# Performance work log

Hardware: AMD Instinct MI355X
Metric: run time of the kernel (lower is better)

## Reference

```python
import jax, jax.numpy as jnp
import numpy as np

NUM_HEADS = 32

def setup_inputs() -> dict:
    key = jax.random.key(0)
    ks = jax.random.split(key, 5)
    B, S, D = 2, 2048, 1024
    d = D // NUM_HEADS  # 32
    return {
        "x": jax.random.normal(ks[0], (B, S, D), dtype=jnp.float32),
        "wq": jax.random.normal(ks[1], (d, d), dtype=jnp.float32) / np.sqrt(d),
        "bq": jnp.zeros((d,), dtype=jnp.float32),
        "wk": jax.random.normal(ks[2], (d, d), dtype=jnp.float32) / np.sqrt(d),
        "bk": jnp.zeros((d,), dtype=jnp.float32),
        "wv": jax.random.normal(ks[3], (d, d), dtype=jnp.float32) / np.sqrt(d),
        "bv": jnp.zeros((d,), dtype=jnp.float32),
        "wo": jax.random.normal(ks[4], (D, D), dtype=jnp.float32) / np.sqrt(D),
        "bo": jnp.zeros((D,), dtype=jnp.float32),
    }

def reference(x, wq, bq, wk, bk, wv, bv, wo, bo):
    B, S, D = x.shape
    H = NUM_HEADS
    d = D // H
    # split heads: [B, S, H, d] -> [B, H, S, d]
    h = x.reshape(B, S, H, d).transpose(0, 2, 1, 3)
    # shared per-head Q/K/V projections (single SelfAttention submodule)
    q = jnp.einsum('bhsd,de->bhse', h, wq) + bq
    k = jnp.einsum('bhsd,de->bhse', h, wk) + bk
    v = jnp.einsum('bhsd,de->bhse', h, wv) + bv
    scale = 1.0 / jnp.sqrt(jnp.asarray(d, dtype=x.dtype))
    scores = jnp.einsum('bhqd,bhkd->bhqk', q, k) * scale  # [B,H,S,S]
    attn = jax.nn.softmax(scores, axis=-1)
    out = jnp.einsum('bhqk,bhkd->bhqd', attn, v)  # [B,H,S,d]
    # concat heads -> [B, S, D]
    concat = out.transpose(0, 2, 1, 3).reshape(B, S, D)
    return concat @ wo + bo
```

## Files before the change

kernel.cpp:

```cpp
#include <hip/hip_runtime.h>
#include <hip/hip_bf16.h>

typedef __attribute__((ext_vector_type(8))) short bf16x8;
typedef __attribute__((ext_vector_type(4))) short bf16x4;
typedef __attribute__((ext_vector_type(4))) float f32x4;

#if defined(__has_builtin)
#if __has_builtin(__builtin_amdgcn_exp2f)
#define EXP2F(x) __builtin_amdgcn_exp2f(x)
#else
#define EXP2F(x) exp2f(x)
#endif
#else
#define EXP2F(x) exp2f(x)
#endif

#define S_LEN 2048
#define NH 32
#define HD 32
#define DMODEL 1024
#define NB 2

static __device__ __forceinline__ unsigned int cvt_pk_bf16(float lo, float hi) {
    unsigned int r;
    asm("v_cvt_pk_bf16_f32 %0, %1, %2" : "=v"(r) : "v"(lo), "v"(hi));
    return r;
}

static __device__ __forceinline__ void mfma16_acc(f32x4& d, bf16x4 a, bf16x4 b) {
    asm("s_nop 2\n\tv_mfma_f32_16x16x16_bf16 %0, %1, %2, %0"
        : "+v"(d) : "v"(a), "v"(b));
}

__global__ __launch_bounds__(256) void qkv_mfma(
    const float* __restrict__ x,
    const float* __restrict__ wq, const float* __restrict__ bq,
    const float* __restrict__ wk, const float* __restrict__ bk,
    const float* __restrict__ wv, const float* __restrict__ bv,
    __hip_bfloat16* __restrict__ qws,
    __hip_bfloat16* __restrict__ kws,
    __hip_bfloat16* __restrict__ vtws)
{
    const int tid = threadIdx.x;
    const int w  = tid >> 6;
    const int ln = tid & 63;
    const int lg = ln >> 4, lm = ln & 15;

    const int bi = blockIdx.x;
    const int tb = bi >> 2;
    const int hq = bi & 3;
    const int t0 = tb * 16;
    const int b  = t0 >> 11;
    const int s0 = t0 & 2047;

    const float SC = 0.1767766953f * 1.44269504089f;

    bf16x8 wqB[2], wkB[2], wvA[2];
    f32x4 bqC[2], bkC[2], bvC[2];
#pragma unroll
    for (int et = 0; et < 2; ++et) {
        const int e = et * 16 + lm;
        union { unsigned int u4[4]; bf16x8 v; } tq, tk, tv;
#pragma unroll
        for (int jj = 0; jj < 4; ++jj) {
            int k0 = lg * 8 + jj * 2;
            tq.u4[jj] = cvt_pk_bf16(wq[k0 * 32 + e] * SC, wq[(k0 + 1) * 32 + e] * SC);
            tk.u4[jj] = cvt_pk_bf16(wk[k0 * 32 + e],      wk[(k0 + 1) * 32 + e]);
            tv.u4[jj] = cvt_pk_bf16(wv[k0 * 32 + e],      wv[(k0 + 1) * 32 + e]);
        }
        wqB[et] = tq.v; wkB[et] = tk.v; wvA[et] = tv.v;

        float bqe = bq[e] * SC;
        float bke = bk[e];
        bqC[et] = (f32x4){bqe, bqe, bqe, bqe};
        bkC[et] = (f32x4){bke, bke, bke, bke};
#pragma unroll
        for (int r = 0; r < 4; ++r)
            bvC[et][r] = bv[et * 16 + lg * 4 + r];
    }

#pragma unroll
    for (int u = 0; u < 2; ++u) {
        const int h = hq * 8 + w * 2 + u;

        const float* xp = x + (size_t)(t0 + lm) * DMODEL + h * 32 + lg * 8;
        float4 xlo = *reinterpret_cast<const float4*>(xp);
        float4 xhi = *reinterpret_cast<const float4*>(xp + 4);
        union { unsigned int u4[4]; bf16x8 v; } xa;
        xa.u4[0] = cvt_pk_bf16(xlo.x, xlo.y);
        xa.u4[1] = cvt_pk_bf16(xlo.z, xlo.w);
        xa.u4[2] = cvt_pk_bf16(xhi.x, xhi.y);
        xa.u4[3] = cvt_pk_bf16(xhi.z, xhi.w);

        const int bh = b * NH + h;
        __hip_bfloat16* qrow = qws + ((size_t)bh * S_LEN + s0) * HD;
        __hip_bfloat16* krow = kws + ((size_t)bh * S_LEN + s0) * HD;
        __hip_bfloat16* vrow = vtws + (size_t)bh * HD * S_LEN + s0;

#pragma unroll
        for (int et = 0; et < 2; ++et) {
            f32x4 qd = __builtin_amdgcn_mfma_f32_16x16x32_bf16(xa.v, wqB[et], bqC[et], 0, 0, 0);
            f32x4 kd = __builtin_amdgcn_mfma_f32_16x16x32_bf16(xa.v, wkB[et], bkC[et], 0, 0, 0);
            f32x4 vd = __builtin_amdgcn_mfma_f32_16x16x32_bf16(wvA[et], xa.v, bvC[et], 0, 0, 0);
#pragma unroll
            for (int r = 0; r < 4; ++r) {
                int srow = 4 * lg + r;
                qrow[(size_t)srow * HD + et * 16 + lm] = __float2bfloat16(qd[r]);
                krow[(size_t)srow * HD + et * 16 + lm] = __float2bfloat16(kd[r]);
                vrow[(size_t)(et * 16 + 4 * lg + r) * S_LEN + lm] = __float2bfloat16(vd[r]);
            }
        }
    }
}

__global__ __launch_bounds__(256) void wo_transpose(
    const float* __restrict__ wo, __hip_bfloat16* __restrict__ wot)
{
    __shared__ float t[64][65];
    const int bx = blockIdx.x;
    const int by = blockIdx.y;
    const int tid = threadIdx.x;
    const int col = tid & 63, row4 = tid >> 6;
#pragma unroll
    for (int i = 0; i < 16; ++i) {
        int r = i * 4 + row4;
        t[r][col] = wo[(size_t)(bx * 64 + r) * DMODEL + by * 64 + col];
    }
    __syncthreads();
#pragma unroll
    for (int i = 0; i < 16; ++i) {
        int r = i * 4 + row4;
        wot[(size_t)(by * 64 + r) * DMODEL + bx * 64 + col] =
            __float2bfloat16(t[col][r]);
    }
}

__global__ __launch_bounds__(256) void attn_kernel(
    const __hip_bfloat16* __restrict__ qws,
    const __hip_bfloat16* __restrict__ kws,
    const __hip_bfloat16* __restrict__ vtws,
    __hip_bfloat16* __restrict__ cws)
{
    const int tid = threadIdx.x;
    const int w  = tid >> 6;
    const int ln = tid & 63;
    const int lg = ln >> 4;
    const int lm = ln & 15;

    const int bi  = blockIdx.x;
    const int xcd = bi & 7;
    const int idx = bi >> 3;
    const int qt  = idx & 31;
    const int bh  = (xcd << 3) | (idx >> 5);
    const int b   = bh >> 5;
    const int h   = bh & 31;

    const __hip_bfloat16* qp = qws + (size_t)bh * S_LEN * HD;
    const char* kpb = (const char*)(kws  + (size_t)bh * S_LEN * HD);
    const char* vpb = (const char*)(vtws + (size_t)bh * HD * S_LEN);

    const int qr0 = qt * 64 + w * 16;

    bf16x8 qb = *reinterpret_cast<const bf16x8*>(qp + (size_t)(qr0 + lm) * HD + lg * 8);

    __shared__ __align__(16) char kv[8192];

    f32x4 l4 = {0.f, 0.f, 0.f, 0.f};
    f32x4 o0 = {0.f, 0.f, 0.f, 0.f};
    f32x4 o1 = {0.f, 0.f, 0.f, 0.f};
    const f32x4 zoff = {-8.f, -8.f, -8.f, -8.f};

    const int vrow  = tid >> 3;
    const int vslot = tid & 7;
    const size_t vsrc = (size_t)vrow * (S_LEN * 2) +
                        (size_t)(vslot ^ (vrow & 7)) * 16;

    int voff[4];
#pragma unroll
    for (int c = 0; c < 4; ++c)
        voff[c] = 4096 + lm * 128 + (((2 * c + (lg >> 1)) ^ (lm & 7)) << 4) + (lg & 1) * 8;

    uint4 kreg = *reinterpret_cast<const uint4*>(kpb + tid * 16);
    uint4 vreg = *reinterpret_cast<const uint4*>(vpb + vsrc);

    for (int kt = 0; kt < S_LEN / 64; ++kt) {
        if (kt) __syncthreads();
        *reinterpret_cast<uint4*>(&kv[tid * 16])        = kreg;
        *reinterpret_cast<uint4*>(&kv[4096 + tid * 16]) = vreg;
        __syncthreads();
        if (kt + 1 < S_LEN / 64) {
            kreg = *reinterpret_cast<const uint4*>(
                kpb + (size_t)(kt + 1) * 4096 + tid * 16);
            vreg = *reinterpret_cast<const uint4*>(
                vpb + vsrc + (size_t)(kt + 1) * 128);
        }

        f32x4 s[4];
#pragma unroll
        for (int c = 0; c < 4; ++c) {
            bf16x8 kf = *reinterpret_cast<const bf16x8*>(
                &kv[c * 1024 + lm * 64 + lg * 16]);
            s[c] = __builtin_amdgcn_mfma_f32_16x16x32_bf16(kf, qb, zoff, 0, 0, 0);
        }

        bf16x4 pb[4];
#pragma unroll
        for (int c = 0; c < 4; ++c) {
            float p0 = EXP2F(s[c][0]);
            float p1 = EXP2F(s[c][1]);
            float p2 = EXP2F(s[c][2]);
            float p3 = EXP2F(s[c][3]);
            l4[0] += p0; l4[1] += p1; l4[2] += p2; l4[3] += p3;
            union { unsigned int u[2]; bf16x4 v; } pk_;
            pk_.u[0] = cvt_pk_bf16(p0, p1);
            pk_.u[1] = cvt_pk_bf16(p2, p3);
            pb[c] = pk_.v;
        }

#pragma unroll
        for (int c = 0; c < 4; ++c) {
            bf16x4 va = *reinterpret_cast<const bf16x4*>(&kv[voff[c]]);
            bf16x4 vb = *reinterpret_cast<const bf16x4*>(&kv[voff[c] + 2048]);
            mfma16_acc(o0, va, pb[c]);
            mfma16_acc(o1, vb, pb[c]);
        }
    }

    asm volatile("s_nop 7\n\ts_nop 7");

    float l = (l4[0] + l4[1]) + (l4[2] + l4[3]);
    l += __shfl_xor(l, 16);
    l += __shfl_xor(l, 32);
    float inv = 1.0f / l;

    __hip_bfloat16* cb = cws + ((size_t)b * S_LEN + qr0 + lm) * DMODEL + h * HD;
    union { unsigned int u[2]; bf16x4 v; } w0, w1;
    w0.u[0] = cvt_pk_bf16(o0[0] * inv, o0[1] * inv);
    w0.u[1] = cvt_pk_bf16(o0[2] * inv, o0[3] * inv);
    w1.u[0] = cvt_pk_bf16(o1[0] * inv, o1[1] * inv);
    w1.u[1] = cvt_pk_bf16(o1[2] * inv, o1[3] * inv);
    *reinterpret_cast<bf16x4*>(cb + lg * 4)      = w0.v;
    *reinterpret_cast<bf16x4*>(cb + 16 + lg * 4) = w1.v;
}

__global__ __launch_bounds__(256) void out_gemm(
    const __hip_bfloat16* __restrict__ A,
    const __hip_bfloat16* __restrict__ Bt,
    const float* __restrict__ bo,
    float* __restrict__ out)
{
    const int tid = threadIdx.x;
    const int ln = tid & 63;
    const int w  = tid >> 6;
    const int lg = ln >> 4, lm = ln & 15;
    const int wr = w >> 1, wc = w & 1;
    const int bi = blockIdx.x;
    const int bn = bi & 7;
    const int bm = bi >> 3;
    const int r0 = bm * 64;
    const int n0 = bn * 128;

    __shared__ __align__(16) char lds[24576];

    f32x4 acc[2][4];
#pragma unroll
    for (int m = 0; m < 2; ++m)
#pragma unroll
        for (int n = 0; n < 4; ++n)
            acc[m][n] = {0.f, 0.f, 0.f, 0.f};

    const int srow = tid >> 3;
    const int sj   = tid & 7;
    const int swo  = srow * 128 + ((sj ^ (srow & 7)) << 4);

    const __hip_bfloat16* Ab = A  + (size_t)r0 * DMODEL;
    const __hip_bfloat16* Bb = Bt + (size_t)n0 * DMODEL;

    uint4 ar0 = *reinterpret_cast<const uint4*>(Ab + (size_t)srow        * DMODEL + sj * 8);
    uint4 ar1 = *reinterpret_cast<const uint4*>(Ab + (size_t)(srow + 32) * DMODEL + sj * 8);
    uint4 br0 = *reinterpret_cast<const uint4*>(Bb + (size_t)srow        * DMODEL + sj * 8);
    uint4 br1 = *reinterpret_cast<const uint4*>(Bb + (size_t)(srow + 32) * DMODEL + sj * 8);
    uint4 br2 = *reinterpret_cast<const uint4*>(Bb + (size_t)(srow + 64) * DMODEL + sj * 8);
    uint4 br3 = *reinterpret_cast<const uint4*>(Bb + (size_t)(srow + 96) * DMODEL + sj * 8);

    for (int k0 = 0; k0 < DMODEL; k0 += 64) {
        if (k0) __syncthreads();
        *reinterpret_cast<uint4*>(&lds[swo])          = ar0;
        *reinterpret_cast<uint4*>(&lds[swo + 4096])   = ar1;
        *reinterpret_cast<uint4*>(&lds[8192 + swo])           = br0;
        *reinterpret_cast<uint4*>(&lds[8192 + swo + 4096])    = br1;
        *reinterpret_cast<uint4*>(&lds[8192 + swo + 8192])    = br2;
        *reinterpret_cast<uint4*>(&lds[8192 + swo + 12288])   = br3;
        __syncthreads();
        if (k0 + 64 < DMODEL) {
            const __hip_bfloat16* An = Ab + k0 + 64;
            const __hip_bfloat16* Bn = Bb + k0 + 64;
            ar0 = *reinterpret_cast<const uint4*>(An + (size_t)srow        * DMODEL + sj * 8);
            ar1 = *reinterpret_cast<const uint4*>(An + (size_t)(srow + 32) * DMODEL + sj * 8);
            br0 = *reinterpret_cast<const uint4*>(Bn + (size_t)srow        * DMODEL + sj * 8);
            br1 = *reinterpret_cast<const uint4*>(Bn + (size_t)(srow + 32) * DMODEL + sj * 8);
            br2 = *reinterpret_cast<const uint4*>(Bn + (size_t)(srow + 64) * DMODEL + sj * 8);
            br3 = *reinterpret_cast<const uint4*>(Bn + (size_t)(srow + 96) * DMODEL + sj * 8);
        }

#pragma unroll
        for (int kh = 0; kh < 2; ++kh) {
            bf16x8 af[2], bf[4];
#pragma unroll
            for (int m = 0; m < 2; ++m) {
                int row = wr * 32 + m * 16 + lm;
                af[m] = *reinterpret_cast<const bf16x8*>(
                    &lds[row * 128 + (((kh * 4 + lg) ^ (row & 7)) << 4)]);
            }
#pragma unroll
            for (int n = 0; n < 4; ++n) {
                int row = wc * 64 + n * 16 + lm;
                bf[n] = *reinterpret_cast<const bf16x8*>(
                    &lds[8192 + row * 128 + (((kh * 4 + lg) ^ (row & 7)) << 4)]);
            }
#pragma unroll
            for (int m = 0; m < 2; ++m)
#pragma unroll
                for (int n = 0; n < 4; ++n)
                    acc[m][n] = __builtin_amdgcn_mfma_f32_16x16x32_bf16(
                        af[m], bf[n], acc[m][n], 0, 0, 0);
        }
    }

#pragma unroll
    for (int n = 0; n < 4; ++n) {
        int col = n0 + wc * 64 + n * 16 + lm;
        float bv = bo[col];
#pragma unroll
        for (int m = 0; m < 2; ++m) {
#pragma unroll
            for (int r = 0; r < 4; ++r) {
                int row = r0 + wr * 32 + m * 16 + lg * 4 + r;
                out[(size_t)row * DMODEL + col] = acc[m][n][r] + bv;
            }
        }
    }
}

extern "C" void kernel_launch(void* const* d_in, const int* in_sizes, int n_in,
                              void* d_out, int out_size, void* d_ws, size_t ws_size,
                              hipStream_t stream)
{
    const float* x  = (const float*)d_in[0];
    const float* wq = (const float*)d_in[1];
    const float* bq = (const float*)d_in[2];
    const float* wk = (const float*)d_in[3];
    const float* bk = (const float*)d_in[4];
    const float* wv = (const float*)d_in[5];
    const float* bv = (const float*)d_in[6];
    const float* wo = (const float*)d_in[7];
    const float* bo = (const float*)d_in[8];
    float* out = (float*)d_out;

    char* ws = (char*)d_ws;
    __hip_bfloat16* qws  = (__hip_bfloat16*)(ws);
    __hip_bfloat16* kws  = (__hip_bfloat16*)(ws + ((size_t)8  << 20));
    __hip_bfloat16* vtws = (__hip_bfloat16*)(ws + ((size_t)16 << 20));
    __hip_bfloat16* cws  = (__hip_bfloat16*)(ws + ((size_t)24 << 20));
    __hip_bfloat16* wot  = (__hip_bfloat16*)(ws + ((size_t)32 << 20));

    qkv_mfma<<<1024, 256, 0, stream>>>(
        x, wq, bq, wk, bk, wv, bv, qws, kws, vtws);
    wo_transpose<<<dim3(16, 16), 256, 0, stream>>>(wo, wot);
    attn_kernel<<<NB * NH * (S_LEN / 64), 256, 0, stream>>>(qws, kws, vtws, cws);
    out_gemm<<<(NB * S_LEN / 64) * (DMODEL / 128), 256, 0, stream>>>(
        cws, wot, bo, out);
}
```

Baseline: 98.38 us.

## Double KV tile per barrier to 128 keys and add MFMA priority hints

The attention loop now stages two 64-key K/V sub-tiles per iteration into a larger shared buffer and processes them back to back. This halves the number of barriers and global-load rounds per key sweep. s_setprio wrappers are also added around the MFMA sections so waves in matrix phases get scheduling priority. The cost is double the LDS per block and more prefetch registers, which may lower occupancy.

```diff
diff --git a/kernel.cpp b/kernel.cpp
--- a/kernel.cpp
+++ b/kernel.cpp
@@ -163,7 +163,7 @@
 
     bf16x8 qb = *reinterpret_cast<const bf16x8*>(qp + (size_t)(qr0 + lm) * HD + lg * 8);
 
-    __shared__ __align__(16) char kv[8192];
+    __shared__ __align__(16) char kv[16384];
 
     f32x4 l4 = {0.f, 0.f, 0.f, 0.f};
     f32x4 o0 = {0.f, 0.f, 0.f, 0.f};
@@ -180,49 +180,68 @@
     for (int c = 0; c < 4; ++c)
         voff[c] = 4096 + lm * 128 + (((2 * c + (lg >> 1)) ^ (lm & 7)) << 4) + (lg & 1) * 8;
 
-    uint4 kreg = *reinterpret_cast<const uint4*>(kpb + tid * 16);
-    uint4 vreg = *reinterpret_cast<const uint4*>(vpb + vsrc);
-
-    for (int kt = 0; kt < S_LEN / 64; ++kt) {
+    const int NT2 = S_LEN / 128;
+
+    uint4 kregA = *reinterpret_cast<const uint4*>(kpb + tid * 16);
+    uint4 vregA = *reinterpret_cast<const uint4*>(vpb + vsrc);
+    uint4 kregB = *reinterpret_cast<const uint4*>(kpb + 4096 + tid * 16);
+    uint4 vregB = *reinterpret_cast<const uint4*>(vpb + vsrc + 128);
+
+    for (int kt = 0; kt < NT2; ++kt) {
         if (kt) __syncthreads();
-        *reinterpret_cast<uint4*>(&kv[tid * 16])        = kreg;
-        *reinterpret_cast<uint4*>(&kv[4096 + tid * 16]) = vreg;
+        *reinterpret_cast<uint4*>(&kv[tid * 16])         = kregA;
+        *reinterpret_cast<uint4*>(&kv[4096 + tid * 16])  = vregA;
+        *reinterpret_cast<uint4*>(&kv[8192 + tid * 16])  = kregB;
+        *reinterpret_cast<uint4*>(&kv[12288 + tid * 16]) = vregB;
         __syncthreads();
-        if (kt + 1 < S_LEN / 64) {
-            kreg = *reinterpret_cast<const uint4*>(
-                kpb + (size_t)(kt + 1) * 4096 + tid * 16);
-            vreg = *reinterpret_cast<const uint4*>(
-                vpb + vsrc + (size_t)(kt + 1) * 128);
-        }
-
-        f32x4 s[4];
-#pragma unroll
-        for (int c = 0; c < 4; ++c) {
-            bf16x8 kf = *reinterpret_cast<const bf16x8*>(
-                &kv[c * 1024 + lm * 64 + lg * 16]);
-            s[c] = __builtin_amdgcn_mfma_f32_16x16x32_bf16(kf, qb, zoff, 0, 0, 0);
-        }
-
-        bf16x4 pb[4];
-#pragma unroll
-        for (int c = 0; c < 4; ++c) {
-            float p0 = EXP2F(s[c][0]);
-            float p1 = EXP2F(s[c][1]);
-            float p2 = EXP2F(s[c][2]);
-            float p3 = EXP2F(s[c][3]);
-            l4[0] += p0; l4[1] += p1; l4[2] += p2; l4[3] += p3;
-            union { unsigned int u[2]; bf16x4 v; } pk_;
-            pk_.u[0] = cvt_pk_bf16(p0, p1);
-            pk_.u[1] = cvt_pk_bf16(p2, p3);
-            pb[c] = pk_.v;
-        }
-
-#pragma unroll
-        for (int c = 0; c < 4; ++c) {
-            bf16x4 va = *reinterpret_cast<const bf16x4*>(&kv[voff[c]]);
-            bf16x4 vb = *reinterpret_cast<const bf16x4*>(&kv[voff[c] + 2048]);
-            mfma16_acc(o0, va, pb[c]);
-            mfma16_acc(o1, vb, pb[c]);
+        if (kt + 1 < NT2) {
+            kregA = *reinterpret_cast<const uint4*>(
+                kpb + (size_t)(kt + 1) * 8192 + tid * 16);
+            vregA = *reinterpret_cast<const uint4*>(
+                vpb + vsrc + (size_t)(kt + 1) * 256);
+            kregB = *reinterpret_cast<const uint4*>(
+                kpb + (size_t)(kt + 1) * 8192 + 4096 + tid * 16);
+            vregB = *reinterpret_cast<const uint4*>(
+                vpb + vsrc + (size_t)(kt + 1) * 256 + 128);
+        }
+
+#pragma unroll
+        for (int sub = 0; sub < 2; ++sub) {
+            const char* base = &kv[sub * 8192];
+
+            f32x4 s[4];
+            __builtin_amdgcn_s_setprio(1);
+#pragma unroll
+            for (int c = 0; c < 4; ++c) {
+                bf16x8 kf = *reinterpret_cast<const bf16x8*>(
+                    base + c * 1024 + lm * 64 + lg * 16);
+                s[c] = __builtin_amdgcn_mfma_f32_16x16x32_bf16(kf, qb, zoff, 0, 0, 0);
+            }
+            __builtin_amdgcn_s_setprio(0);
+
+            bf16x4 pb[4];
+#pragma unroll
+            for (int c = 0; c < 4; ++c) {
+                float p0 = EXP2F(s[c][0]);
+                float p1 = EXP2F(s[c][1]);
+                float p2 = EXP2F(s[c][2]);
+                float p3 = EXP2F(s[c][3]);
+                l4[0] += p0; l4[1] += p1; l4[2] += p2; l4[3] += p3;
+                union { unsigned int u[2]; bf16x4 v; } pk_;
+                pk_.u[0] = cvt_pk_bf16(p0, p1);
+                pk_.u[1] = cvt_pk_bf16(p2, p3);
+                pb[c] = pk_.v;
+            }
+
+            __builtin_amdgcn_s_setprio(1);
+#pragma unroll
+            for (int c = 0; c < 4; ++c) {
+                bf16x4 va = *reinterpret_cast<const bf16x4*>(base + voff[c]);
+                bf16x4 vb = *reinterpret_cast<const bf16x4*>(base + voff[c] + 2048);
+                mfma16_acc(o0, va, pb[c]);
+                mfma16_acc(o1, vb, pb[c]);
+            }
+            __builtin_amdgcn_s_setprio(0);
         }
     }
 
```

After: 97.85 us. About the same (-0.5%).
